# Performance work log

Measured on AMD Instinct MI355X. Metric: run time of the kernel, lower is better.

The kernel has to match this reference:

```python
import jax, jax.numpy as jnp
import numpy as np


def setup_inputs() -> dict:
    key = jax.random.key(0)
    k0, k1, k2, k3 = jax.random.split(key, 4)
    B, H, W, C, h = 2, 64, 64, 256, 8
    N = H * W
    # per-pixel, per-head (dy, dx) match offsets; a few pixels of displacement
    max_offset = jax.random.normal(k0, (B, N, h, 2), dtype=jnp.float32) * 4.0
    q = jax.random.normal(k1, (B, N, C), dtype=jnp.float32)
    k = jax.random.normal(k2, (B, N, C), dtype=jnp.float32)
    v = jax.random.normal(k3, (B, N, C), dtype=jnp.float32)
    return {"max_offset": max_offset, "q": q, "k": k, "v": v,
            "H": H, "W": W, "r_h": 3, "r_w": 3}


def reference(max_offset, q, k, v, H, W, r_h, r_w):
    """MatchAttention fused forward (l1_norm, scale=1.0).

    Each query pixel (y,x), head g attends to a (2*r_h+1)x(2*r_w+1) window
    centered at (y,x) + round(max_offset[...,g]), clamped to the image.
    Similarity is the negative L1 distance between q and gathered k.
    Returns (output [B,N,C], attn_out [B,N,h,K]).
    """
    B, N, C = q.shape
    h = max_offset.shape[2]
    Ch = C // h
    scale = 1.0
    attn_type = "l1_norm"  # fixed; 'l2_norm' would use squared distance

    # window deltas, K = (2*r_h+1)*(2*r_w+1)
    dy = jnp.arange(-r_h, r_h + 1)
    dx = jnp.arange(-r_w, r_w + 1)
    gy, gx = jnp.meshgrid(dy, dx, indexing="ij")
    ddy, ddx = gy.reshape(-1), gx.reshape(-1)  # [K]

    ys = (jnp.arange(N) // W)[None, :, None]  # [1,N,1]
    xs = (jnp.arange(N) % W)[None, :, None]

    off = jnp.round(max_offset).astype(jnp.int32)  # [B,N,h,2] (dy,dx)
    cy = ys + off[..., 0]                          # [B,N,h] window center
    cx = xs + off[..., 1]
    py = jnp.clip(cy[..., None] + ddy, 0, H - 1)   # [B,N,h,K]
    px = jnp.clip(cx[..., None] + ddx, 0, W - 1)
    idx = py * W + px                              # flat pixel index, [B,N,h,K]

    # split heads and move head axis forward: [B,h,N,Ch]
    qh = q.reshape(B, N, h, Ch).transpose(0, 2, 1, 3)
    kh = k.reshape(B, N, h, Ch).transpose(0, 2, 1, 3)
    vh = v.reshape(B, N, h, Ch).transpose(0, 2, 1, 3)
    idx_t = idx.transpose(0, 2, 1, 3)              # [B,h,N,K]

    # gather windows: [B,h,N,K,Ch]
    gather = jax.vmap(jax.vmap(lambda tbl, i: tbl[i]))
    kg = gather(kh, idx_t)
    vg = gather(vh, idx_t)

    # negative L1 distance similarity, softmax over window
    sim = -scale * jnp.abs(qh[:, :, :, None, :] - kg).sum(-1)  # [B,h,N,K]
    attn = jax.nn.softmax(sim, axis=-1)

    out = jnp.einsum("bhnk,bhnkc->bhnc", attn, vg)
    output = out.transpose(0, 2, 1, 3).reshape(B, N, C)
    attn_out = attn.transpose(0, 2, 1, 3)          # [B,N,h,K]
    return output, attn_out
```

## Files before the change

### kernel.cpp

```cpp
#include <hip/hip_runtime.h>
#include <hip/hip_fp16.h>
#include <math.h>

constexpr int B = 2, H = 64, W = 64, C = 256, NH = 8, CH = 32;
constexpr int R = 3, KW = 7, KK = 49, N = H * W;
constexpr int PIX = 32;

template <int CTRL>
static __device__ __forceinline__ float dpp_mov(float v) {
  union { float f; int i; } u;
  u.f = v;
  u.i = __builtin_amdgcn_update_dpp(u.i, u.i, CTRL, 0xf, 0xf, true);
  return u.f;
}
#define DPP_QUAD_XOR1 0xB1
#define DPP_QUAD_XOR2 0x4E
#define DPP_HALF_MIRROR 0x141

__global__ void __launch_bounds__(256) pack_kv_kernel(
    const float* __restrict__ kp, const float* __restrict__ vp,
    __half* __restrict__ kv) {
  const int idx = blockIdx.x * 256 + threadIdx.x;
  const int e8 = idx & 7;
  const int g = (idx >> 3) & 7;
  const int bn = idx >> 6;
  const float4 kf = *(const float4*)(kp + (size_t)bn * C + g * CH + e8 * 4);
  const float4 vf = *(const float4*)(vp + (size_t)bn * C + g * CH + e8 * 4);
  __half2 o[4];
  o[0] = __floats2half2_rn(kf.x, kf.y);
  o[1] = __floats2half2_rn(kf.z, kf.w);
  o[2] = __floats2half2_rn(vf.x, vf.y);
  o[3] = __floats2half2_rn(vf.z, vf.w);
  *(float4*)(kv + ((size_t)(bn * NH + g) * 64 + e8 * 8)) = *(float4*)o;
}

union KV { float4 f; __half2 h[4]; };

__global__ void __launch_bounds__(256, 2) match_attn_kernel(
    const float* __restrict__ moff, const float* __restrict__ qp,
    const __half* __restrict__ kvp, float* __restrict__ outp,
    float* __restrict__ attnp) {
  const int t = threadIdx.x;
  const int e8 = t & 7;
  const int p = t >> 3;

  const int xcd = blockIdx.x & 7;
  const int rest = blockIdx.x >> 3;
  const int bg = xcd * 2 + (rest >> 7);
  const int slot = rest & 127;
  const int y = slot >> 1;
  const int x = (slot & 1) * PIX + p;
  const int g = bg & 7;
  const int b = bg >> 3;
  const int n = y * W + x;

  const float2 off = *(const float2*)(moff + ((size_t)(b * N + n) * NH + g) * 2);
  const int cy = y + (int)rintf(off.x);
  const int cx = x + (int)rintf(off.y);

  int pxo[KW];
#pragma unroll
  for (int i = 0; i < KW; ++i) pxo[i] = min(max(cx + i - R, 0), W - 1) << 10;
  const char* kvimg = (const char*)kvp +
      (size_t)b * N * NH * 128 + g * 128 + e8 * 16;

  const int chn = g * CH + e8 * 4;
  const float4 q0 = *(const float4*)(qp + (size_t)(b * N + n) * C + chn);
  const __half2 q01 = __floats2half2_rn(q0.x, q0.y);
  const __half2 q23 = __floats2half2_rn(q0.z, q0.w);

  float ev7[KW];
#pragma unroll
  for (int i = 0; i < KW; ++i) ev7[i] = 0.f;
  float4 acc = {0.f, 0.f, 0.f, 0.f};
  float d0 = 0.f, d1 = 0.f;

#define ROWOFF(iy) (min(max(cy + (iy) - R, 0), H - 1) << 16)
#define LOADROW(buf, iy)                                            \
  {                                                                 \
    const int _ro = ROWOFF(iy);                                     \
    _Pragma("unroll") for (int ix = 0; ix < KW; ++ix)               \
        buf[ix].f = *(const float4*)(kvimg + (_ro + pxo[ix]));      \
  }
#define COMPROW(buf, iy)                                            \
  {                                                                 \
    const bool _own = ((iy) == e8);                                 \
    _Pragma("unroll") for (int ix = 0; ix < KW; ++ix) {             \
      const __half2 d01h = __habs2(__hsub2(q01, buf[ix].h[0]));     \
      const __half2 d23h = __habs2(__hsub2(q23, buf[ix].h[1]));     \
      const float2 f01 = __half22float2(d01h);                      \
      const float2 f23 = __half22float2(d23h);                      \
      float s = (f01.x + f01.y) + (f23.x + f23.y);                  \
      s += dpp_mov<DPP_QUAD_XOR1>(s);                               \
      s += dpp_mov<DPP_QUAD_XOR2>(s);                               \
      s += dpp_mov<DPP_HALF_MIRROR>(s);                             \
      const float e = __expf(-s);  \
      if (ix & 1) d1 += e; else d0 += e;                            \
      if (_own) ev7[ix] = e;                                        \
      const float2 v01 = __half22float2(buf[ix].h[2]);              \
      const float2 v23 = __half22float2(buf[ix].h[3]);              \
      acc.x += e * v01.x; acc.y += e * v01.y;                       \
      acc.z += e * v23.x; acc.w += e * v23.y;                       \
    }                                                               \
  }

  KV A[KW], Bf[KW];
  LOADROW(A, 0)
#pragma clang loop unroll(disable)
  for (int ty = 0; ty < KW - 1; ty += 2) {
    LOADROW(Bf, ty + 1)
    COMPROW(A, ty)
    LOADROW(A, ty + 2)
    COMPROW(Bf, ty + 1)
  }
  COMPROW(A, KW - 1)

  const float inv = 1.0f / (d0 + d1);
  float4 o;
  o.x = acc.x * inv; o.y = acc.y * inv; o.z = acc.z * inv; o.w = acc.w * inv;
  *(float4*)(outp + (size_t)(b * N + n) * C + chn) = o;

  if (e8 < KW) {
    float* attn_row = attnp + ((size_t)(b * N + n) * NH + g) * KK + e8 * KW;
#pragma unroll
    for (int ix = 0; ix < KW; ++ix) attn_row[ix] = ev7[ix] * inv;
  }
}

extern "C" void kernel_launch(void* const* d_in, const int* in_sizes, int n_in,
                              void* d_out, int out_size, void* d_ws, size_t ws_size,
                              hipStream_t stream) {
  const float* moff = (const float*)d_in[0];
  const float* q    = (const float*)d_in[1];
  const float* k    = (const float*)d_in[2];
  const float* v    = (const float*)d_in[3];
  float* out  = (float*)d_out;
  float* attn = out + (size_t)B * N * C;
  __half* kv = (__half*)d_ws;

  pack_kv_kernel<<<B * N * NH * 8 / 256, 256, 0, stream>>>(k, v, kv);
  const int grid = B * NH * N / PIX;
  match_attn_kernel<<<grid, 256, 0, stream>>>(moff, q, kv, out, attn);
}
```

Before: 112.5 us.

## Triple-buffer KV row loads, use exp2 with prescaled fp16, fdot2 reductions, raise occupancy

The main loop moves from double-buffered to triple-buffered row loads, so two rows of K/V gathers are in flight while one row is computed. K and q are prescaled by log2(e) before conversion to fp16, which lets the native exp2 instruction replace __expf. The per-lane L1 partial sum now uses fdot2 against a vector of ones, and the V accumulation uses explicit fmaf. Launch bounds ask for 4 blocks per CU instead of 2, which limits registers and risks spills given the larger buffer set. Prescaling before fp16 rounding slightly changes numerics.

After: 174.2 us. 1.55x slower.

```diff
diff --git a/kernel.cpp b/kernel.cpp
--- a/kernel.cpp
+++ b/kernel.cpp
@@ -5,6 +5,9 @@
 constexpr int B = 2, H = 64, W = 64, C = 256, NH = 8, CH = 32;
 constexpr int R = 3, KW = 7, KK = 49, N = H * W;
 constexpr int PIX = 32;
+constexpr float LOG2E = 1.4426950408889634f;
+
+typedef _Float16 h16x2 __attribute__((ext_vector_type(2)));
 
 template <int CTRL>
 static __device__ __forceinline__ float dpp_mov(float v) {
@@ -17,6 +20,12 @@
 #define DPP_QUAD_XOR2 0x4E
 #define DPP_HALF_MIRROR 0x141
 
+static __device__ __forceinline__ h16x2 h2n(__half2 x) {
+  union { __half2 h; h16x2 n; } u;
+  u.h = x;
+  return u.n;
+}
+
 __global__ void __launch_bounds__(256) pack_kv_kernel(
     const float* __restrict__ kp, const float* __restrict__ vp,
     __half* __restrict__ kv) {
@@ -27,16 +36,16 @@
   const float4 kf = *(const float4*)(kp + (size_t)bn * C + g * CH + e8 * 4);
   const float4 vf = *(const float4*)(vp + (size_t)bn * C + g * CH + e8 * 4);
   __half2 o[4];
-  o[0] = __floats2half2_rn(kf.x, kf.y);
-  o[1] = __floats2half2_rn(kf.z, kf.w);
+  o[0] = __floats2half2_rn(kf.x * LOG2E, kf.y * LOG2E);
+  o[1] = __floats2half2_rn(kf.z * LOG2E, kf.w * LOG2E);
   o[2] = __floats2half2_rn(vf.x, vf.y);
   o[3] = __floats2half2_rn(vf.z, vf.w);
   *(float4*)(kv + ((size_t)(bn * NH + g) * 64 + e8 * 8)) = *(float4*)o;
 }
 
-union KV { float4 f; __half2 h[4]; };
+union KV { float4 f; __half2 h[4]; h16x2 n[4]; };
 
-__global__ void __launch_bounds__(256, 2) match_attn_kernel(
+__global__ void __launch_bounds__(256, 4) match_attn_kernel(
     const float* __restrict__ moff, const float* __restrict__ qp,
     const __half* __restrict__ kvp, float* __restrict__ outp,
     float* __restrict__ attnp) {
@@ -61,13 +70,15 @@
   int pxo[KW];
 #pragma unroll
   for (int i = 0; i < KW; ++i) pxo[i] = min(max(cx + i - R, 0), W - 1) << 10;
-  const char* kvimg = (const char*)kvp +
-      (size_t)b * N * NH * 128 + g * 128 + e8 * 16;
+  const char* __restrict__ kvb =
+      (const char*)kvp + (size_t)(b * N * NH + g) * 128;
+  const int lane16 = e8 * 16;
 
   const int chn = g * CH + e8 * 4;
   const float4 q0 = *(const float4*)(qp + (size_t)(b * N + n) * C + chn);
-  const __half2 q01 = __floats2half2_rn(q0.x, q0.y);
-  const __half2 q23 = __floats2half2_rn(q0.z, q0.w);
+  const __half2 q01 = __floats2half2_rn(q0.x * LOG2E, q0.y * LOG2E);
+  const __half2 q23 = __floats2half2_rn(q0.z * LOG2E, q0.w * LOG2E);
+  const h16x2 one2 = {(_Float16)1.0f, (_Float16)1.0f};
 
   float ev7[KW];
 #pragma unroll
@@ -75,43 +86,46 @@
   float4 acc = {0.f, 0.f, 0.f, 0.f};
   float d0 = 0.f, d1 = 0.f;
 
-#define ROWOFF(iy) (min(max(cy + (iy) - R, 0), H - 1) << 16)
-#define LOADROW(buf, iy)                                            \
-  {                                                                 \
-    const int _ro = ROWOFF(iy);                                     \
-    _Pragma("unroll") for (int ix = 0; ix < KW; ++ix)               \
-        buf[ix].f = *(const float4*)(kvimg + (_ro + pxo[ix]));      \
+#define ROWBASE(iy) ((min(max(cy + (iy)-R, 0), H - 1) << 16) + lane16)
+#define LOADROW(buf, iy)                                      \
+  {                                                           \
+    const int _rb = ROWBASE(iy);                              \
+    _Pragma("unroll") for (int ix = 0; ix < KW; ++ix)         \
+        buf[ix].f = *(const float4*)(kvb + (_rb + pxo[ix]));  \
   }
-#define COMPROW(buf, iy)                                            \
-  {                                                                 \
-    const bool _own = ((iy) == e8);                                 \
-    _Pragma("unroll") for (int ix = 0; ix < KW; ++ix) {             \
-      const __half2 d01h = __habs2(__hsub2(q01, buf[ix].h[0]));     \
-      const __half2 d23h = __habs2(__hsub2(q23, buf[ix].h[1]));     \
-      const float2 f01 = __half22float2(d01h);                      \
-      const float2 f23 = __half22float2(d23h);                      \
-      float s = (f01.x + f01.y) + (f23.x + f23.y);                  \
-      s += dpp_mov<DPP_QUAD_XOR1>(s);                               \
-      s += dpp_mov<DPP_QUAD_XOR2>(s);                               \
-      s += dpp_mov<DPP_HALF_MIRROR>(s);                             \
-      const float e = __expf(-s);  \
-      if (ix & 1) d1 += e; else d0 += e;                            \
-      if (_own) ev7[ix] = e;                                        \
-      const float2 v01 = __half22float2(buf[ix].h[2]);              \
-      const float2 v23 = __half22float2(buf[ix].h[3]);              \
-      acc.x += e * v01.x; acc.y += e * v01.y;                       \
-      acc.z += e * v23.x; acc.w += e * v23.y;                       \
-    }                                                               \
+#define COMPROW(buf, iy)                                                     \
+  {                                                                          \
+    const bool _own = ((iy) == e8);                                          \
+    _Pragma("unroll") for (int ix = 0; ix < KW; ++ix) {                      \
+      const h16x2 d01 = h2n(__habs2(__hsub2(q01, buf[ix].h[0])));            \
+      const h16x2 d23 = h2n(__habs2(__hsub2(q23, buf[ix].h[1])));            \
+      float s = __builtin_amdgcn_fdot2(                                      \
+          d01, one2, __builtin_amdgcn_fdot2(d23, one2, 0.0f, false), false); \
+      s += dpp_mov<DPP_QUAD_XOR1>(s);                                        \
+      s += dpp_mov<DPP_QUAD_XOR2>(s);                                        \
+      s += dpp_mov<DPP_HALF_MIRROR>(s);                                      \
+      const float e = __builtin_amdgcn_exp2f(-s);  \
+      if (ix & 1) d1 += e; else d0 += e;                                     \
+      if (_own) ev7[ix] = e;                                                 \
+      const h16x2 v01 = buf[ix].n[2], v23 = buf[ix].n[3];                    \
+      acc.x = fmaf(e, (float)v01.x, acc.x);                                  \
+      acc.y = fmaf(e, (float)v01.y, acc.y);                                  \
+      acc.z = fmaf(e, (float)v23.x, acc.z);                                  \
+      acc.w = fmaf(e, (float)v23.y, acc.w);                                  \
+    }                                                                        \
   }
 
-  KV A[KW], Bf[KW];
+  KV A[KW], Bf[KW], Cf[KW];
   LOADROW(A, 0)
+  LOADROW(Bf, 1)
 #pragma clang loop unroll(disable)
-  for (int ty = 0; ty < KW - 1; ty += 2) {
-    LOADROW(Bf, ty + 1)
+  for (int ty = 0; ty < KW - 3; ty += 3) {
+    LOADROW(Cf, ty + 2)
     COMPROW(A, ty)
-    LOADROW(A, ty + 2)
+    LOADROW(A, ty + 3)
     COMPROW(Bf, ty + 1)
+    if (ty + 4 < KW) LOADROW(Bf, ty + 4)
+    COMPROW(Cf, ty + 2)
   }
   COMPROW(A, KW - 1)
 
```
